# Kernel tuning notes

Measured on AMD Instinct MI355X. Metric: run time of the kernel, lower is better.

The kernel has to match this reference:

```python
import jax, jax.numpy as jnp
import numpy as np

B, L, D, K = 8, 4096, 1024, 256

def setup_inputs() -> dict:
    key = jax.random.key(0)
    k1, k2, k3, k4 = jax.random.split(key, 4)
    x = jax.random.normal(k1, (B, L, D), dtype=jnp.float32)
    W_qkv = jax.random.normal(k2, (D, 3 * D), dtype=jnp.float32) * 0.02
    b_qkv = jnp.zeros((3 * D,), dtype=jnp.float32)
    H_k = jax.random.normal(k3, (L, K), dtype=jnp.float32)
    H_v = jax.random.normal(k4, (L, K), dtype=jnp.float32)
    return {"x": x, "W_qkv": W_qkv, "b_qkv": b_qkv, "H_k": H_k, "H_v": H_v}

def reference(x, W_qkv, b_qkv, H_k, H_v):
    Bn, Ln, Dn = x.shape
    qkv = x @ W_qkv + b_qkv                       # [B,L,3D]
    q, k, v = jnp.split(qkv, 3, axis=-1)          # each [B,L,D]
    K_proj = jnp.einsum('lk,bld->bkd', H_k, k)    # [B,K,D]
    V_proj = jnp.einsum('lk,bld->bkd', H_v, v)    # [B,K,D]
    scores = jnp.einsum('bld,bkd->blk', q, K_proj) / jnp.sqrt(jnp.asarray(Dn, x.dtype))
    weights = jax.nn.softmax(scores, axis=-1)     # [B,L,K]
    out = jnp.einsum('blk,bkd->bld', weights, V_proj)
    return out
```

## Files before the change

kernel.cpp:

```cpp
#include <hip/hip_runtime.h>


typedef __attribute__((ext_vector_type(8))) _Float16 half8;
typedef __attribute__((ext_vector_type(4))) _Float16 half4;
typedef __attribute__((ext_vector_type(4))) float f32x4;

#define AS1 __attribute__((address_space(1)))
#define AS3 __attribute__((address_space(3)))

__device__ __forceinline__ void gld_lds16(const void* g, void* l) {
    __builtin_amdgcn_global_load_lds((AS1 void*)g, (AS3 void*)l, 16, 0, 0);
}

template <typename T> struct is_f32 { static constexpr bool v = false; };
template <> struct is_f32<float> { static constexpr bool v = true; };

template <typename T> __device__ __forceinline__ T to_out(float v);
template <> __device__ __forceinline__ float    to_out<float>(float v) { return v; }
template <> __device__ __forceinline__ _Float16 to_out<_Float16>(float v) { return (_Float16)v; }

__device__ __forceinline__ half8 cvt_h8(f32x4 a, f32x4 b) {
    half8 h;
    h[0] = (_Float16)a[0]; h[1] = (_Float16)a[1]; h[2] = (_Float16)a[2]; h[3] = (_Float16)a[3];
    h[4] = (_Float16)b[0]; h[5] = (_Float16)b[1]; h[6] = (_Float16)b[2]; h[7] = (_Float16)b[3];
    return h;
}

template <typename OUT_T, bool SWIZ>
__global__ __launch_bounds__(256) void gemm_bt(
    const _Float16* __restrict__ A, long sA0, long sA1, long sA2, int lda,
    const _Float16* __restrict__ B, long sB0, long sB1, long sB2, int ldb,
    OUT_T* __restrict__ C, long sC0, long sC1, long sC2, int ldc,
    int nz0, int nz1, int NM, int NN, int Kd,
    const float* __restrict__ bias, long sb0,
    const float* __restrict__ rowv, const float* __restrict__ colv, float scale)
{
    {
        const int z = blockIdx.z;
        const int z0 = z % nz0, t = z / nz0, z1 = t % nz1, z2 = t / nz1;
        A += z0 * sA0 + z1 * sA1 + z2 * sA2;
        B += z0 * sB0 + z1 * sB1 + z2 * sB2;
        C += z0 * sC0 + z1 * sC1 + z2 * sC2;
        if (bias) bias += (long)z0 * sb0;
    }
    int mb, nb;
    if (SWIZ) {
        const int g = blockIdx.x, r = g % (8 * NN);
        mb = (g / (8 * NN)) * 8 + (r & 7);
        nb = r >> 3;
    } else {
        mb = blockIdx.x % NM;
        nb = blockIdx.x / NM;
    }
    const int tid = threadIdx.x, w = tid >> 6, ln = tid & 63;
    const int wm = (w >> 1) * 64, wn = (w & 1) * 64;

    __shared__ __attribute__((aligned(16))) _Float16 As[128 * 64];
    __shared__ __attribute__((aligned(16))) _Float16 Bs[128 * 64];

    f32x4 acc[4][4] = {};

    const int cb0 = w * 256;
    const _Float16* Ablk = A + (long)mb * 128 * lda;
    const _Float16* Bblk = B + (long)nb * 128 * ldb;

    const int lr = ln & 15, rs = ln & 7, kq = ln >> 4;

    for (int k0 = 0; k0 < Kd; k0 += 64) {
#pragma unroll
        for (int t = 0; t < 4; ++t) {
            const int ci = cb0 + t * 64 + ln;
            const int r = ci >> 3, kc = (ci & 7) ^ (r & 7);
            gld_lds16(Ablk + (long)r * lda + k0 + kc * 8, &As[(cb0 + t * 64) * 8]);
            gld_lds16(Bblk + (long)r * ldb + k0 + kc * 8, &Bs[(cb0 + t * 64) * 8]);
        }
        __syncthreads();
#pragma unroll
        for (int kh = 0; kh < 2; ++kh) {
            const int c = (((kh * 4) + kq) ^ rs) * 8;
            half8 af[4], bf[4];
#pragma unroll
            for (int i = 0; i < 4; ++i) {
                af[i] = *(const half8*)&As[(wm + i * 16 + lr) * 64 + c];
                bf[i] = *(const half8*)&Bs[(wn + i * 16 + lr) * 64 + c];
            }
#pragma unroll
            for (int i = 0; i < 4; ++i)
#pragma unroll
                for (int j = 0; j < 4; ++j)
                    acc[i][j] = __builtin_amdgcn_mfma_f32_16x16x32_f16(af[i], bf[j], acc[i][j], 0, 0, 0);
        }
        __syncthreads();
    }

    const int crow = mb * 128 + wm + (kq << 2);
    const int ccol = nb * 128 + wn + lr;
#pragma unroll
    for (int i = 0; i < 4; ++i)
#pragma unroll
        for (int r = 0; r < 4; ++r) {
            const long row = crow + i * 16 + r;
#pragma unroll
            for (int j = 0; j < 4; ++j) {
                const int col = ccol + j * 16;
                float v = acc[i][j][r] * scale;
                if (bias) v += bias[col];
                if (rowv) v += rowv[row] * colv[col];
                if constexpr (is_f32<OUT_T>::v)
                    __builtin_nontemporal_store(v, &C[row * ldc + col]);
                else
                    C[row * ldc + col] = to_out<OUT_T>(v);
            }
        }
}

__global__ __launch_bounds__(256) void gemm_tn_pkv(
    const float* __restrict__ X, const float* __restrict__ Hk,
    const float* __restrict__ Hv, float* __restrict__ P32)
{
    const int z = blockIdx.z, b = z & 7, ks = z >> 3;
    const int mb = blockIdx.x & 7, nb = blockIdx.x >> 3;
    const float* Ab = X + (long)b * 4194304 + (long)ks * 2097152 + mb * 128;
    const float* Bb = (nb >= 2 ? Hv + (nb - 2) * 128 : Hk + nb * 128) + (long)ks * 524288;
    float* Cb = P32 + (long)ks * 4194304 + (long)b * 524288;

    const int tid = threadIdx.x, w = tid >> 6, ln = tid & 63;
    const int wm = (w >> 1) * 64, wn = (w & 1) * 64;
    const int lr = ln & 15, rs = ln & 7, kq = ln >> 4;
    const int skq = (tid >> 2) & 7;
    const int sm0 = ((tid & 3) | ((tid >> 5) << 2)) * 4;

    __shared__ __attribute__((aligned(16))) _Float16 As[128 * 64];
    __shared__ __attribute__((aligned(16))) _Float16 Bs[128 * 64];

    f32x4 acc[4][4] = {};
    f32x4 va[8], vb[8];

#pragma unroll
    for (int i = 0; i < 8; ++i)
        va[i] = *(const f32x4*)(Ab + (long)(skq * 8 + i) * 1024 + sm0);
#pragma unroll
    for (int i = 0; i < 8; ++i)
        vb[i] = *(const f32x4*)(Bb + (long)(skq * 8 + i) * 256 + sm0);

    for (int k0 = 0; k0 < 2048; k0 += 64) {
#pragma unroll
        for (int j = 0; j < 4; ++j) {
            half8 h;
#pragma unroll
            for (int i = 0; i < 8; ++i) h[i] = (_Float16)va[i][j];
            *(half8*)&As[(sm0 + j) * 64 + ((skq ^ ((sm0 + j) & 7)) << 3)] = h;
        }
#pragma unroll
        for (int j = 0; j < 4; ++j) {
            half8 h;
#pragma unroll
            for (int i = 0; i < 8; ++i) h[i] = (_Float16)vb[i][j];
            *(half8*)&Bs[(sm0 + j) * 64 + ((skq ^ ((sm0 + j) & 7)) << 3)] = h;
        }
        __syncthreads();
        if (k0 + 64 < 2048) {
            const long kn = k0 + 64;
#pragma unroll
            for (int i = 0; i < 8; ++i)
                va[i] = *(const f32x4*)(Ab + (kn + skq * 8 + i) * 1024 + sm0);
#pragma unroll
            for (int i = 0; i < 8; ++i)
                vb[i] = *(const f32x4*)(Bb + (kn + skq * 8 + i) * 256 + sm0);
        }
#pragma unroll
        for (int kh = 0; kh < 2; ++kh) {
            const int c = (((kh * 4) + kq) ^ rs) * 8;
            half8 af[4], bf[4];
#pragma unroll
            for (int i = 0; i < 4; ++i) {
                af[i] = *(const half8*)&As[(wm + i * 16 + lr) * 64 + c];
                bf[i] = *(const half8*)&Bs[(wn + i * 16 + lr) * 64 + c];
            }
#pragma unroll
            for (int i = 0; i < 4; ++i)
#pragma unroll
                for (int j = 0; j < 4; ++j)
                    acc[i][j] = __builtin_amdgcn_mfma_f32_16x16x32_f16(af[i], bf[j], acc[i][j], 0, 0, 0);
        }
        __syncthreads();
    }

    const int crow = mb * 128 + wm + (kq << 2);
    const int ccol = nb * 128 + wn + lr;
#pragma unroll
    for (int i = 0; i < 4; ++i)
#pragma unroll
        for (int j = 0; j < 4; ++j)
            *(f32x4*)&Cb[(long)(ccol + j * 16) * 1024 + crow + i * 16] = acc[i][j];
}

__global__ void reduce_kv2(const float* __restrict__ P, _Float16* __restrict__ Pkv) {
    const long o = ((long)blockIdx.x * 256 + threadIdx.x) * 4;
    float4 a = *(const float4*)(P + o);
    float4 bb = *(const float4*)(P + o + 4194304);
    half4 out;
    out[0] = (_Float16)(a.x + bb.x); out[1] = (_Float16)(a.y + bb.y);
    out[2] = (_Float16)(a.z + bb.z); out[3] = (_Float16)(a.w + bb.w);
    *(half4*)(Pkv + o) = out;
}

__global__ __launch_bounds__(256) void score_softmax(
    const float* __restrict__ X, const _Float16* __restrict__ Bm,
    const float* __restrict__ cb, _Float16* __restrict__ Wts)
{
    const int b = blockIdx.z, mb = blockIdx.x;
    const float* Ab = X + (long)b * 4194304 + (long)mb * 131072;
    const _Float16* Bb = Bm + (long)b * 262144;
    const int tid = threadIdx.x, w = tid >> 6, ln = tid & 63;
    const int lr = ln & 15, rs = ln & 7, kq = ln >> 4;

    __shared__ __attribute__((aligned(16))) _Float16 SM[24576];
    _Float16* As = SM;
    _Float16* Bs = SM + 8192;

    f32x4 acc[2][16] = {};

    for (int k0 = 0; k0 < 1024; k0 += 64) {
        f32x4 pa[4][2];
#pragma unroll
        for (int t = 0; t < 4; ++t) {
            const int ci = w * 256 + t * 64 + ln;
            const int r = ci >> 3, kc = (ci & 7) ^ (r & 7);
            const float* ap = Ab + (long)r * 1024 + k0 + kc * 8;
            pa[t][0] = *(const f32x4*)ap;
            pa[t][1] = *(const f32x4*)(ap + 4);
        }
#pragma unroll
        for (int t = 0; t < 8; ++t) {
            const int cbase = w * 512 + t * 64;
            const int ci = cbase + ln, r = ci >> 3, kc = (ci & 7) ^ (r & 7);
            gld_lds16(Bb + (long)r * 1024 + k0 + kc * 8, &Bs[cbase * 8]);
        }
#pragma unroll
        for (int t = 0; t < 4; ++t) {
            const int ci = w * 256 + t * 64 + ln;
            *(half8*)&As[ci * 8] = cvt_h8(pa[t][0], pa[t][1]);
        }
        __syncthreads();
#pragma unroll
        for (int kh = 0; kh < 2; ++kh) {
            const int c = (((kh * 4) + kq) ^ rs) * 8;
            const half8 af0 = *(const half8*)&As[(w * 32 + lr) * 64 + c];
            const half8 af1 = *(const half8*)&As[(w * 32 + 16 + lr) * 64 + c];
#pragma unroll
            for (int j = 0; j < 16; ++j) {
                const half8 bf = *(const half8*)&Bs[(j * 16 + lr) * 64 + c];
                acc[0][j] = __builtin_amdgcn_mfma_f32_16x16x32_f16(af0, bf, acc[0][j], 0, 0, 0);
                acc[1][j] = __builtin_amdgcn_mfma_f32_16x16x32_f16(af1, bf, acc[1][j], 0, 0, 0);
            }
        }
        __syncthreads();
    }

    float cbl[16];
    const float* cbb = cb + b * 256;
#pragma unroll
    for (int j = 0; j < 16; ++j) cbl[j] = cbb[j * 16 + lr];

#pragma unroll
    for (int i = 0; i < 2; ++i)
#pragma unroll
        for (int r = 0; r < 4; ++r) {
            float m = -3.0e38f;
#pragma unroll
            for (int j = 0; j < 16; ++j) {
                float v = acc[i][j][r] + cbl[j];
                acc[i][j][r] = v;
                m = fmaxf(m, v);
            }
            m = fmaxf(m, __shfl_xor(m, 1, 64)); m = fmaxf(m, __shfl_xor(m, 2, 64));
            m = fmaxf(m, __shfl_xor(m, 4, 64)); m = fmaxf(m, __shfl_xor(m, 8, 64));
            float s = 0.f;
#pragma unroll
            for (int j = 0; j < 16; ++j) {
                float e = __expf(acc[i][j][r] - m);
                acc[i][j][r] = e;
                s += e;
            }
            s += __shfl_xor(s, 1, 64); s += __shfl_xor(s, 2, 64);
            s += __shfl_xor(s, 4, 64); s += __shfl_xor(s, 8, 64);
            const float inv = 1.0f / s;
#pragma unroll
            for (int j = 0; j < 16; ++j) acc[i][j][r] *= inv;
        }

#pragma unroll
    for (int i = 0; i < 2; ++i) {
        __syncthreads();
#pragma unroll
        for (int r = 0; r < 4; ++r)
#pragma unroll
            for (int j = 0; j < 16; ++j)
                SM[(w * 16 + kq * 4 + r) * 264 + j * 16 + lr] = (_Float16)acc[i][j][r];
        __syncthreads();
#pragma unroll
        for (int u = 0; u < 8; ++u) {
            const int idx = tid + 256 * u, row = idx >> 5, ci2 = idx & 31;
            const half8 v = *(const half8*)&SM[row * 264 + ci2 * 8];
            const long grow = (long)b * 4096 + mb * 128 + (row >> 4) * 32 + i * 16 + (row & 15);
            *(half8*)&Wts[grow * 256 + ci2 * 8] = v;
        }
    }
}

__global__ __launch_bounds__(256) void tr64(const float* __restrict__ src,
                                            _Float16* __restrict__ dst,
                                            _Float16* __restrict__ dsth,
                                            int R, int C, long sbatch, long dbatch) {
    __shared__ float T[64 * 65];
    const float* s = src + (long)blockIdx.z * sbatch;
    _Float16* d = dst + (long)blockIdx.z * dbatch;
    _Float16* dh = dsth ? dsth + (long)blockIdx.z * sbatch : nullptr;
    const int c0 = blockIdx.x * 64, r0 = blockIdx.y * 64;
    const int t = threadIdx.x;
    {
        const int row = t >> 2, cp = (t & 3) * 16;
        const float* sp = s + (long)(r0 + row) * C + c0 + cp;
        const float4 v0 = *(const float4*)(sp + 0);
        const float4 v1 = *(const float4*)(sp + 4);
        const float4 v2 = *(const float4*)(sp + 8);
        const float4 v3 = *(const float4*)(sp + 12);
        float* Tr = &T[row * 65 + cp];
        Tr[ 0] = v0.x; Tr[ 1] = v0.y; Tr[ 2] = v0.z; Tr[ 3] = v0.w;
        Tr[ 4] = v1.x; Tr[ 5] = v1.y; Tr[ 6] = v1.z; Tr[ 7] = v1.w;
        Tr[ 8] = v2.x; Tr[ 9] = v2.y; Tr[10] = v2.z; Tr[11] = v2.w;
        Tr[12] = v3.x; Tr[13] = v3.y; Tr[14] = v3.z; Tr[15] = v3.w;
        if (dh) {
            half8 h0, h1;
            h0[0] = (_Float16)v0.x; h0[1] = (_Float16)v0.y;
            h0[2] = (_Float16)v0.z; h0[3] = (_Float16)v0.w;
            h0[4] = (_Float16)v1.x; h0[5] = (_Float16)v1.y;
            h0[6] = (_Float16)v1.z; h0[7] = (_Float16)v1.w;
            h1[0] = (_Float16)v2.x; h1[1] = (_Float16)v2.y;
            h1[2] = (_Float16)v2.z; h1[3] = (_Float16)v2.w;
            h1[4] = (_Float16)v3.x; h1[5] = (_Float16)v3.y;
            h1[6] = (_Float16)v3.z; h1[7] = (_Float16)v3.w;
            _Float16* dp = dh + (long)(r0 + row) * C + c0 + cp;
            *(half8*)(dp + 0) = h0;
            *(half8*)(dp + 8) = h1;
        }
    }
    __syncthreads();
    {
        const int qq = t & 7, cc = t >> 3;
#pragma unroll
        for (int it = 0; it < 2; ++it) {
            const int col = cc + it * 32;
            half8 o;
#pragma unroll
            for (int u = 0; u < 8; ++u) o[u] = (_Float16)T[(qq * 8 + u) * 65 + col];
            *(half8*)(d + (long)(c0 + col) * R + r0 + qq * 8) = o;
        }
    }
}

__global__ void colsum2(const float* __restrict__ Hk, const float* __restrict__ Hv,
                        float* __restrict__ sk, float* __restrict__ sv) {
    const float* H = blockIdx.y ? Hv : Hk;
    float* s = blockIdx.y ? sv : sk;
    const int c = threadIdx.x;
    const long r0 = (long)blockIdx.x * 64;
    float acc = 0.f;
    for (int r = 0; r < 64; ++r) acc += H[(r0 + r) * 256 + c];
    atomicAdd(s + c, acc);
}

__global__ void bias_vecs(const float* __restrict__ W, const float* __restrict__ b,
                          float* __restrict__ gh) {
    const int wid = blockIdx.x * 4 + (threadIdx.x >> 6);
    const int ln = threadIdx.x & 63;
    float acc = 0.f;
    if (wid < 1024) {
        for (int j = 0; j < 16; ++j) { int d = ln + 64 * j; acc += b[d] * W[(long)wid * 3072 + 1024 + d]; }
    } else if (wid < 2048) {
        for (int j = 0; j < 16; ++j) { int d = ln + 64 * j; acc += b[1024 + d] * W[(long)(wid - 1024) * 3072 + d]; }
    } else if (wid == 2048) {
        for (int j = 0; j < 16; ++j) { int d = ln + 64 * j; acc += b[d] * b[1024 + d]; }
    } else return;
#pragma unroll
    for (int o = 32; o > 0; o >>= 1) acc += __shfl_xor(acc, o, 64);
    if (!ln) gh[wid] = acc * 0.03125f;
}

__global__ void cb_kernel(const _Float16* __restrict__ Pk, const float* __restrict__ gh,
                          const float* __restrict__ sk, float* __restrict__ cb) {
    const int wid = blockIdx.x * 4 + (threadIdx.x >> 6);
    const int ln = threadIdx.x & 63;
    const _Float16* row = Pk + (long)(wid >> 8) * 524288 + (long)(wid & 255) * 1024;
    float acc = 0.f;
    for (int j = 0; j < 16; ++j) { int c = ln + 64 * j; acc += (float)row[c] * gh[c]; }
#pragma unroll
    for (int o = 32; o > 0; o >>= 1) acc += __shfl_xor(acc, o, 64);
    if (!ln) cb[wid] = acc + sk[wid & 255] * gh[2048];
}

extern "C" void kernel_launch(void* const* d_in, const int* in_sizes, int n_in,
                              void* d_out, int out_size, void* d_ws, size_t ws_size,
                              hipStream_t stream) {
    const float* x    = (const float*)d_in[0];
    const float* Wq   = (const float*)d_in[1];
    const float* bqkv = (const float*)d_in[2];
    const float* Hk   = (const float*)d_in[3];
    const float* Hv   = (const float*)d_in[4];
    float* out = (float*)d_out;

    char* p = (char*)d_ws;
    auto take = [&](size_t n) { char* r = p; p += (n + 255) & ~(size_t)255; return r; };
    _Float16* Wt  = (_Float16*)take(3145728ull * 2);
    _Float16* Wh  = (_Float16*)take(3145728ull * 2);
    _Float16* Pkv = (_Float16*)take(4194304ull * 2);
    _Float16* VpT = (_Float16*)take(2097152ull * 2);
    _Float16* Gt  = (_Float16*)take(1048576ull * 2);
    _Float16* Mt  = (_Float16*)take(2097152ull * 2);
    float*    gh  = (float*)take(2049 * 4);
    float*    sk  = (float*)take(512 * 4);
    float*    sv  = sk + 256;
    float*    cbv = (float*)take(2048 * 4);
    float*    P32 = (float*)take(8388608ull * 4);
    _Float16* wts = (_Float16*)take(8388608ull * 2);

    const dim3 B256(256);

    tr64<<<dim3(48, 16, 1), B256, 0, stream>>>(Wq, Wt, Wh, 1024, 3072, 0, 0);
    hipMemsetAsync(sk, 0, 512 * 4, stream);
    colsum2<<<dim3(64, 2, 1), B256, 0, stream>>>(Hk, Hv, sk, sv);
    bias_vecs<<<513, B256, 0, stream>>>(Wq, bqkv, gh);

    gemm_tn_pkv<<<dim3(32, 1, 16), B256, 0, stream>>>(x, Hk, Hv, P32);
    reduce_kv2<<<4096, B256, 0, stream>>>(P32, Pkv);

    gemm_bt<_Float16, true><<<dim3(64, 1, 1), B256, 0, stream>>>(
        Wh, 0, 0, 0, 3072, Wh + 1024, 0, 0, 0, 3072, Gt, 0, 0, 0, 1024,
        1, 1, 8, 8, 1024, nullptr, 0, nullptr, nullptr, 1.0f);
    gemm_bt<_Float16, true><<<dim3(16, 1, 8), B256, 0, stream>>>(
        Wt + 2097152, 0, 0, 0, 1024, Pkv + 262144, 524288, 0, 0, 1024,
        VpT, 262144, 0, 0, 256,
        8, 1, 8, 2, 1024, nullptr, 0, bqkv + 2048, sv, 1.0f);
    gemm_bt<_Float16, false><<<dim3(16, 1, 8), B256, 0, stream>>>(
        Pkv, 524288, 0, 0, 1024, Gt, 0, 0, 0, 1024,
        Mt, 262144, 0, 0, 1024,
        8, 1, 2, 8, 1024, nullptr, 0, sk, gh + 1024, 0.03125f);
    cb_kernel<<<512, B256, 0, stream>>>(Pkv, gh, sk, cbv);
    score_softmax<<<dim3(32, 1, 8), B256, 0, stream>>>(x, Mt, cbv, wts);
    gemm_bt<float, true><<<dim3(256, 1, 8), B256, 0, stream>>>(
        wts, 1048576, 0, 0, 256, VpT, 262144, 0, 0, 256,
        out, 4194304, 0, 0, 1024,
        8, 1, 32, 8, 256, nullptr, 0, nullptr, nullptr, 1.0f);
}
```

Before: 468.2 us.

## Double-buffer LDS in K/V projection GEMM with two-stage register prefetch

Changes the pkv GEMM mainloop to use two LDS buffers so that staging the next tile (fp32-to-fp16 convert plus LDS write) and issuing global loads two tiles ahead overlap with the MFMA work on the current buffer. This removes one __syncthreads per iteration. LDS use doubles to 64KB per block, which may lower occupancy, and register pressure may rise.

```diff
diff --git a/kernel.cpp b/kernel.cpp
--- a/kernel.cpp
+++ b/kernel.cpp
@@ -114,6 +114,27 @@
         }
 }
 
+#define PKV_LOADA(KK)                                                          \
+    _Pragma("unroll") for (int i = 0; i < 8; ++i)                              \
+        va[i] = *(const f32x4*)(Ab + ((long)(KK) + skq * 8 + i) * 1024 + sm0);
+#define PKV_LOADB(KK)                                                          \
+    _Pragma("unroll") for (int i = 0; i < 8; ++i)                              \
+        vb[i] = *(const f32x4*)(Bb + ((long)(KK) + skq * 8 + i) * 256 + sm0);
+#define PKV_STAGE(BUF)                                                         \
+    {                                                                          \
+        const int so = (BUF) << 13;                                            \
+        _Pragma("unroll") for (int j = 0; j < 4; ++j) {                        \
+            half8 h;                                                           \
+            _Pragma("unroll") for (int i = 0; i < 8; ++i) h[i] = (_Float16)va[i][j]; \
+            *(half8*)&As[so + (sm0 + j) * 64 + ((skq ^ ((sm0 + j) & 7)) << 3)] = h; \
+        }                                                                      \
+        _Pragma("unroll") for (int j = 0; j < 4; ++j) {                        \
+            half8 h;                                                           \
+            _Pragma("unroll") for (int i = 0; i < 8; ++i) h[i] = (_Float16)vb[i][j]; \
+            *(half8*)&Bs[so + (sm0 + j) * 64 + ((skq ^ ((sm0 + j) & 7)) << 3)] = h; \
+        }                                                                      \
+    }
+
 __global__ __launch_bounds__(256) void gemm_tn_pkv(
     const float* __restrict__ X, const float* __restrict__ Hk,
     const float* __restrict__ Hv, float* __restrict__ P32)
@@ -130,52 +151,30 @@
     const int skq = (tid >> 2) & 7;
     const int sm0 = ((tid & 3) | ((tid >> 5) << 2)) * 4;
 
-    __shared__ __attribute__((aligned(16))) _Float16 As[128 * 64];
-    __shared__ __attribute__((aligned(16))) _Float16 Bs[128 * 64];
+    __shared__ __attribute__((aligned(16))) _Float16 As[2 * 128 * 64];
+    __shared__ __attribute__((aligned(16))) _Float16 Bs[2 * 128 * 64];
 
     f32x4 acc[4][4] = {};
     f32x4 va[8], vb[8];
 
-#pragma unroll
-    for (int i = 0; i < 8; ++i)
-        va[i] = *(const f32x4*)(Ab + (long)(skq * 8 + i) * 1024 + sm0);
-#pragma unroll
-    for (int i = 0; i < 8; ++i)
-        vb[i] = *(const f32x4*)(Bb + (long)(skq * 8 + i) * 256 + sm0);
-
-    for (int k0 = 0; k0 < 2048; k0 += 64) {
-#pragma unroll
-        for (int j = 0; j < 4; ++j) {
-            half8 h;
-#pragma unroll
-            for (int i = 0; i < 8; ++i) h[i] = (_Float16)va[i][j];
-            *(half8*)&As[(sm0 + j) * 64 + ((skq ^ ((sm0 + j) & 7)) << 3)] = h;
-        }
-#pragma unroll
-        for (int j = 0; j < 4; ++j) {
-            half8 h;
-#pragma unroll
-            for (int i = 0; i < 8; ++i) h[i] = (_Float16)vb[i][j];
-            *(half8*)&Bs[(sm0 + j) * 64 + ((skq ^ ((sm0 + j) & 7)) << 3)] = h;
-        }
-        __syncthreads();
-        if (k0 + 64 < 2048) {
-            const long kn = k0 + 64;
-#pragma unroll
-            for (int i = 0; i < 8; ++i)
-                va[i] = *(const f32x4*)(Ab + (kn + skq * 8 + i) * 1024 + sm0);
-#pragma unroll
-            for (int i = 0; i < 8; ++i)
-                vb[i] = *(const f32x4*)(Bb + (kn + skq * 8 + i) * 256 + sm0);
-        }
+    PKV_LOADA(0) PKV_LOADB(0)
+    PKV_STAGE(0)
+    PKV_LOADA(64) PKV_LOADB(64)
+
+    const int NT = 32;
+    for (int t = 0; t < NT; ++t) {
+        __syncthreads();
+        if (t + 1 < NT) PKV_STAGE((t + 1) & 1)
+        if (t + 2 < NT) { PKV_LOADA((t + 2) * 64) PKV_LOADB((t + 2) * 64) }
+        const int bo = (t & 1) << 13;
 #pragma unroll
         for (int kh = 0; kh < 2; ++kh) {
             const int c = (((kh * 4) + kq) ^ rs) * 8;
             half8 af[4], bf[4];
 #pragma unroll
             for (int i = 0; i < 4; ++i) {
-                af[i] = *(const half8*)&As[(wm + i * 16 + lr) * 64 + c];
-                bf[i] = *(const half8*)&Bs[(wn + i * 16 + lr) * 64 + c];
+                af[i] = *(const half8*)&As[bo + (wm + i * 16 + lr) * 64 + c];
+                bf[i] = *(const half8*)&Bs[bo + (wn + i * 16 + lr) * 64 + c];
             }
 #pragma unroll
             for (int i = 0; i < 4; ++i)
@@ -183,7 +182,6 @@
                 for (int j = 0; j < 4; ++j)
                     acc[i][j] = __builtin_amdgcn_mfma_f32_16x16x32_f16(af[i], bf[j], acc[i][j], 0, 0, 0);
         }
-        __syncthreads();
     }
 
     const int crow = mb * 128 + wm + (kq << 2);
```

Result: no change. 469.9 us (+0.3%).
